# Optimization experiments

Measured on AMD Instinct MI355X. Metric: run time of the kernel, lower is better.

Reference implementation:

```python
import math
import jax, jax.numpy as jnp
import numpy as np

B, T, C = 256, 200, 512
H = 8
N_ATTN = 512
HEAD = N_ATTN // H          # 64
ROT = HEAD // 2             # 32 (rotary_ndims = head_size * 0.5)
MAXLEN = 200
ITEM_NUM = 100000


def setup_inputs() -> dict:
    key = jax.random.key(0)
    ks = jax.random.split(key, 16)
    s = 0.02
    item_emb = jax.random.normal(ks[0], (ITEM_NUM + 1, C), jnp.float32) * s
    item_emb = item_emb.at[0].set(0.0)  # padding_idx=0
    inp = {
        "user_ids": jax.random.randint(ks[1], (B,), 0, 10000),
        "log_seqs": jax.random.randint(ks[2], (B, T), 0, ITEM_NUM + 1),
        "pos_seqs": jax.random.randint(ks[3], (B, T), 0, ITEM_NUM + 1),
        "neg_seqs": jax.random.randint(ks[4], (B, T), 0, ITEM_NUM + 1),
        "item_emb": item_emb,
        "time_w": 1.0 + jax.random.normal(ks[5], (H, MAXLEN), jnp.float32) * 0.1,
        "time_alpha": 1.0 + jax.random.normal(ks[6], (H, 1, MAXLEN), jnp.float32) * 0.1,
        "time_beta": 1.0 + jax.random.normal(ks[7], (H, MAXLEN, 1), jnp.float32) * 0.1,
        "time_gamma": 1.0 + jax.random.normal(ks[8], (MAXLEN, 1), jnp.float32) * 0.1,
        "Wq": jax.random.normal(ks[9], (N_ATTN, C), jnp.float32) * s,
        "bq": jnp.zeros((N_ATTN,), jnp.float32),
        "Wk": jax.random.normal(ks[10], (N_ATTN, C), jnp.float32) * s,
        "bk": jnp.zeros((N_ATTN,), jnp.float32),
        "Wv": jax.random.normal(ks[11], (N_ATTN, C), jnp.float32) * s,
        "bv": jnp.zeros((N_ATTN,), jnp.float32),
        "Wmix": jax.random.normal(ks[12], (H, H), jnp.float32) * (1.0 / math.sqrt(H)),
        "Wo": jax.random.normal(ks[13], (C, N_ATTN), jnp.float32) * s,
        "bo": jnp.zeros((C,), jnp.float32),
    }
    return inp


def _rotate_half(x):
    x1, x2 = x[..., : x.shape[-1] // 2], x[..., x.shape[-1] // 2 :]
    return jnp.concatenate((-x2, x1), axis=-1)


def _mha_pro(x_items, time_w, time_alpha, time_beta, time_gamma,
             Wq, bq, Wk, bk, Wv, bv, Wmix, Wo, bo):
    # x_items: [B, T, C]
    TT = MAXLEN
    # Toeplitz time-decay matrix built exactly like the torch pad/tile/reshape trick
    w = jnp.pad(time_w, ((0, 0), (0, TT)))          # [H, 2TT]
    w = jnp.tile(w, (1, TT))                         # [H, 2TT*TT]
    w = w[:, :-TT].reshape(H, TT, 2 * TT - 1)        # [H, TT, 2TT-1]
    w = w[:, :, TT - 1 :]                            # [H, TT, TT]
    w = w[:, :T, :T] * time_alpha[:, :, :T] * time_beta[:, :T, :]  # [H, T, T]

    # time_shift: shift first half of channels down by one token
    half = C // 2
    shifted = jnp.pad(x_items[:, :, :half], ((0, 0), (1, 0), (0, 0)))[:, :-1]
    x = jnp.concatenate([shifted, x_items[:, :, half:]], axis=-1)  # [B, T, C]

    q = (x @ Wq.T + bq).reshape(B, T, H, HEAD).transpose(0, 2, 1, 3)  # [B,H,T,D]
    k = (x @ Wk.T + bk).reshape(B, T, H, HEAD).transpose(0, 2, 1, 3)
    v = (x @ Wv.T + bv).reshape(B, T, H, HEAD).transpose(0, 2, 1, 3)

    # partial rotary on first ROT dims
    q_rot, q_pass = q[..., :ROT], q[..., ROT:]
    k_rot, k_pass = k[..., :ROT], k[..., ROT:]
    inv_freq = 1.0 / (10000.0 ** (jnp.arange(0, ROT, 2, dtype=jnp.float32) / ROT))
    freqs = jnp.arange(T, dtype=jnp.float32)[:, None] * inv_freq[None, :]  # [T, ROT/2]
    emb = jnp.concatenate((freqs, freqs), axis=-1)   # [T, ROT]
    cos, sin = jnp.cos(emb), jnp.sin(emb)
    q_rot = q_rot * cos + _rotate_half(q_rot) * sin
    k_rot = k_rot * cos + _rotate_half(k_rot) * sin
    q = jnp.concatenate((q_rot, q_pass), axis=-1)
    k = jnp.concatenate((k_rot, k_pass), axis=-1)

    att = jnp.einsum('bhtd,bhsd->bhts', q, k) * (1.0 / math.sqrt(HEAD))
    causal = jnp.tril(jnp.ones((T, T), bool))
    att = jnp.where(causal, att, -jnp.inf)
    att = jax.nn.softmax(att, axis=-1)
    att = att * w                                   # learned time-decay mask
    att = jnp.einsum('hg,bgts->bhts', Wmix, att)    # 1x1 conv across heads

    out = jnp.einsum('bhts,bhsd->bhtd', att, v)
    out = out.transpose(0, 2, 1, 3).reshape(B, T, N_ATTN)
    out = (out @ Wo.T + bo) * time_gamma[:T, :]
    return out


def reference(user_ids, log_seqs, pos_seqs, neg_seqs, item_emb,
              time_w, time_alpha, time_beta, time_gamma,
              Wq, bq, Wk, bk, Wv, bv, Wmix, Wo, bo):
    x_items = item_emb[log_seqs]                    # [B, T, C]
    log_feats = _mha_pro(x_items, time_w, time_alpha, time_beta, time_gamma,
                         Wq, bq, Wk, bk, Wv, bv, Wmix, Wo, bo)
    pos_embs = item_emb[pos_seqs]
    neg_embs = item_emb[neg_seqs]
    pos_logits = log_feats * pos_embs               # [B, T, C] (as in source)
    neg_logits = (log_feats * neg_embs).sum(axis=-1)  # [B, T]
    return pos_logits, neg_logits
```

## Files before the change

kernel.cpp:

```cpp
#include <hip/hip_runtime.h>

#define B_    256
#define T_    200
#define C_    512
#define H_    8
#define HEAD_ 64
#define M_    (B_ * T_)
#define POS_OUT_ (M_ * C_)
#define QK_ROWS_ 208
#define VT_PAD_  224
#define P_PAD_   200

typedef __attribute__((ext_vector_type(8))) _Float16 f16x8;
typedef __attribute__((ext_vector_type(4))) _Float16 f16x4;
typedef __attribute__((ext_vector_type(2))) _Float16 f16x2;
typedef __attribute__((ext_vector_type(4))) float f32x4;

__device__ __forceinline__ void gload16(const void* g, void* l) {
    __builtin_amdgcn_global_load_lds(
        (const __attribute__((address_space(1))) unsigned int*)g,
        (__attribute__((address_space(3))) unsigned int*)l, 16, 0, 0);
}

__global__ __launch_bounds__(256) void gather_shift_k(
    const float* __restrict__ emb, const int* __restrict__ logs,
    _Float16* __restrict__ x)
{
    int bt = blockIdx.x;
    int t  = bt % T_;
    int tid = threadIdx.x;
    int c  = tid * 2;
    _Float16* xr = x + (size_t)bt * C_;
    if (c < 256) {
        if (t == 0) {
            *(f16x2*)(xr + c) = (f16x2){(_Float16)0.0f, (_Float16)0.0f};
        } else {
            int id_prev = logs[bt - 1];
            float2 v = *(const float2*)(emb + (size_t)id_prev * C_ + c);
            *(f16x2*)(xr + c) = (f16x2){(_Float16)v.x, (_Float16)v.y};
        }
    } else {
        int id_cur = logs[bt];
        float2 v = *(const float2*)(emb + (size_t)id_cur * C_ + c);
        *(f16x2*)(xr + c) = (f16x2){(_Float16)v.x, (_Float16)v.y};
    }
}

__global__ __launch_bounds__(256) void convert_w_k(
    const float* __restrict__ Wq, const float* __restrict__ Wk,
    const float* __restrict__ Wv, const float* __restrict__ Wo,
    _Float16* __restrict__ dst)
{
    int idx = blockIdx.x * 256 + threadIdx.x;
    int mat = idx >> 16;
    int off = (idx & 65535) << 2;
    const float* src = (mat == 0) ? Wq : (mat == 1) ? Wk : (mat == 2) ? Wv : Wo;
    float4 v = *(const float4*)(src + off);
    f16x4 o = { (_Float16)v.x, (_Float16)v.y, (_Float16)v.z, (_Float16)v.w };
    *(f16x4*)(dst + ((size_t)mat << 18) + off) = o;
}

__global__ __launch_bounds__(256) void wtab_k(
    const float* __restrict__ tw, const float* __restrict__ ta,
    const float* __restrict__ tb, float* __restrict__ wtab)
{
    int idx = blockIdx.x * 256 + threadIdx.x;
    int g   = idx / (208 * 208);
    int rem = idx % (208 * 208);
    int t = rem / 208, s = rem % 208;
    int tt = min(t, 199), ss = min(s, 199);
    int wi = min(max(199 - tt + ss, 0), 199);
    wtab[idx] = tw[g * 200 + wi] * ta[g * 200 + ss] * tb[g * 200 + tt];
}

__global__ __launch_bounds__(256) void zero_neg_k(float* __restrict__ out)
{
    out[(size_t)POS_OUT_ + blockIdx.x * 256 + threadIdx.x] = 0.0f;
}

__global__ __launch_bounds__(256) void zero_pads_k(
    _Float16* __restrict__ Qb, _Float16* __restrict__ Kb,
    _Float16* __restrict__ Vt)
{
    int bh = blockIdx.x;
    int tid = threadIdx.x;
    for (int idx = tid; idx < 8 * 64; idx += 256) {
        Qb[(size_t)bh * QK_ROWS_ * 64 + 200 * 64 + idx] = (_Float16)0.0f;
        Kb[(size_t)bh * QK_ROWS_ * 64 + 200 * 64 + idx] = (_Float16)0.0f;
    }
    for (int idx = tid; idx < 64 * (VT_PAD_ - 200); idx += 256) {
        int d = idx / (VT_PAD_ - 200), s = 200 + idx % (VT_PAD_ - 200);
        Vt[(size_t)bh * 64 * VT_PAD_ + (size_t)d * VT_PAD_ + s] = (_Float16)0.0f;
    }
}

__global__ __launch_bounds__(256) void gemm_qkv_k(
    const _Float16* __restrict__ xh,
    const _Float16* __restrict__ Wh,
    const float* __restrict__ bq, const float* __restrict__ bk, const float* __restrict__ bv,
    _Float16* __restrict__ Qb, _Float16* __restrict__ Kb,
    _Float16* __restrict__ Vt,
    int nmt)
{
    int n = blockIdx.x;
    int mt, v;
    if ((nmt & 7) == 0) { int q8 = n & 7, i = n >> 3; mt = (i / 12) * 8 + q8; v = i % 12; }
    else               { mt = n / 12; v = n % 12; }
    int which = v >> 2;
    int nt    = v & 3;
    int m0    = mt * 128;
    const _Float16* Wm = Wh + ((size_t)(which * 4 + nt) * 128) * 512;
    const float* bias = (which == 0) ? bq : (which == 1) ? bk : bv;

    __shared__ _Float16 As[3][128 * 32];
    __shared__ _Float16 Bs[3][128 * 32];

    int tid  = threadIdx.x;
    int w    = tid >> 6, lane = tid & 63;
    int quad = lane >> 4, l15 = lane & 15;
    int wm   = w >> 1,    wn  = w & 1;
    int srow = lane >> 2, scg = lane & 3;
    int scg_src = scg ^ ((srow >> 1) & 3);
    int rq = (l15 >> 1) & 3;

    auto stage = [&](int buf, int k0) {
#pragma unroll
        for (int rr = 0; rr < 2; ++rr) {
            int seg = rr * 4 + w;
            int row = seg * 16 + srow;
            gload16(xh + (size_t)(m0 + row) * 512 + k0 + scg_src * 8, As[buf] + seg * 512);
            gload16(Wm + (size_t)row * 512 + k0 + scg_src * 8, Bs[buf] + seg * 512);
        }
    };

    f32x4 acc[4][4];
#pragma unroll
    for (int m = 0; m < 4; ++m)
#pragma unroll
        for (int nn = 0; nn < 4; ++nn) acc[m][nn] = (f32x4){0.f, 0.f, 0.f, 0.f};

    stage(0, 0);
    stage(1, 32);
#pragma unroll
    for (int s = 0; s < 16; ++s) {
        if (s < 15) asm volatile("s_waitcnt vmcnt(4)" ::: "memory");
        else        asm volatile("s_waitcnt vmcnt(0)" ::: "memory");
        __builtin_amdgcn_s_barrier();
        __builtin_amdgcn_sched_barrier(0);
        const _Float16* Ab = As[s % 3];
        const _Float16* Bb = Bs[s % 3];
        f16x8 af[4], bf[4];
#pragma unroll
        for (int m = 0; m < 4; ++m)
            af[m] = *(const f16x8*)(Ab + (wm * 4 + m) * 512 + l15 * 32 + (quad ^ rq) * 8);
#pragma unroll
        for (int nn = 0; nn < 4; ++nn)
            bf[nn] = *(const f16x8*)(Bb + (wn * 4 + nn) * 512 + l15 * 32 + (quad ^ rq) * 8);
        if (s <= 13) stage((s + 2) % 3, (s + 2) * 32);
#pragma unroll
        for (int m = 0; m < 4; ++m)
#pragma unroll
            for (int nn = 0; nn < 4; ++nn)
                acc[m][nn] = __builtin_amdgcn_mfma_f32_16x16x32_f16(af[m], bf[nn], acc[m][nn], 0, 0, 0);
    }

    int h = nt * 2 + wn;
    if (which < 2) {
        _Float16* dst = (which == 0) ? Qb : Kb;
        float sc = (which == 0) ? 0.125f : 1.0f;
        float invf = powf(10000.0f, -(float)l15 / 16.0f);
#pragma unroll
        for (int m = 0; m < 4; ++m) {
#pragma unroll
            for (int r = 0; r < 4; ++r) {
                int row = m0 + wm * 64 + m * 16 + quad * 4 + r;
                int bl = row / T_, t = row % T_;
                float sn, cs;
                __sincosf((float)t * invf, &sn, &cs);
                size_t base = ((size_t)(bl * 8 + h) * QK_ROWS_ + t) * 64;
                float av = acc[m][0][r] + bias[h * 64 + l15];
                float bv2 = acc[m][1][r] + bias[h * 64 + 16 + l15];
                dst[base + l15]      = (_Float16)((av * cs - bv2 * sn) * sc);
                dst[base + 16 + l15] = (_Float16)((bv2 * cs + av * sn) * sc);
                dst[base + 32 + l15] = (_Float16)((acc[m][2][r] + bias[h * 64 + 32 + l15]) * sc);
                dst[base + 48 + l15] = (_Float16)((acc[m][3][r] + bias[h * 64 + 48 + l15]) * sc);
            }
        }
    } else {
#pragma unroll
        for (int nn = 0; nn < 4; ++nn) {
            int ch = nn * 16 + l15;
            float bval = bias[h * 64 + ch];
#pragma unroll
            for (int m = 0; m < 4; ++m) {
                int r0 = m0 + wm * 64 + m * 16 + quad * 4;
                int t0v = r0 % T_;
                if (t0v <= 196) {
                    int bl = r0 / T_;
                    f16x4 v4 = {(_Float16)(acc[m][nn][0] + bval),
                                (_Float16)(acc[m][nn][1] + bval),
                                (_Float16)(acc[m][nn][2] + bval),
                                (_Float16)(acc[m][nn][3] + bval)};
                    *(f16x4*)(Vt + ((size_t)(bl * 8 + h) * 64 + ch) * VT_PAD_ + t0v) = v4;
                } else {
#pragma unroll
                    for (int r = 0; r < 4; ++r) {
                        int rw = r0 + r;
                        int bl = rw / T_, s = rw % T_;
                        Vt[((size_t)(bl * 8 + h) * 64 + ch) * VT_PAD_ + s] = (_Float16)(acc[m][nn][r] + bval);
                    }
                }
            }
        }
    }
}

__global__ __launch_bounds__(512, 4) void attn_fused_k(
    const _Float16* __restrict__ Qb, const _Float16* __restrict__ Kb,
    const _Float16* __restrict__ Vt,
    const float* __restrict__ wtab,
    const float* __restrict__ wmix,
    _Float16* __restrict__ ao)
{
    int n    = blockIdx.x;
    int xcd  = n & 7, slot = n >> 3;
    int i_tile = 12 - (slot % 13);
    int b      = (slot / 13) * 8 + xcd;

    int tid  = threadIdx.x;
    int wave = tid >> 6, lane = tid & 63;
    int quad = lane >> 4, l15 = lane & 15;
    int t0   = i_tile * 16;
    int nst  = i_tile + 1;
    int smax = nst * 16;
    int lim  = smax < 200 ? smax : 200;

    __shared__ _Float16 Pt[8][16][P_PAD_];
    __shared__ float mixs[64];

    if (tid < 64) mixs[tid] = wmix[tid];

    {
        int g = wave;
        const _Float16* Qg = Qb + (size_t)(b * 8 + g) * QK_ROWS_ * 64;
        const _Float16* Kg = Kb + (size_t)(b * 8 + g) * QK_ROWS_ * 64;
        f16x8 a0 = *(const f16x8*)(Qg + (size_t)(t0 + l15) * 64 + quad * 8);
        f16x8 a1 = *(const f16x8*)(Qg + (size_t)(t0 + l15) * 64 + quad * 8 + 32);

        f32x4 sf[13];
        __builtin_amdgcn_s_setprio(1);
#pragma unroll
        for (int st = 0; st < 13; ++st) if (st < nst) {
            f16x8 k0 = *(const f16x8*)(Kg + (size_t)(st * 16 + l15) * 64 + quad * 8);
            f16x8 k1 = *(const f16x8*)(Kg + (size_t)(st * 16 + l15) * 64 + quad * 8 + 32);
            f32x4 c = {0.f, 0.f, 0.f, 0.f};
            c = __builtin_amdgcn_mfma_f32_16x16x32_f16(a0, k0, c, 0, 0, 0);
            c = __builtin_amdgcn_mfma_f32_16x16x32_f16(a1, k1, c, 0, 0, 0);
            sf[st] = c;
        }
        __builtin_amdgcn_s_setprio(0);
        float inv[4];
#pragma unroll
        for (int r = 0; r < 4; ++r) {
            int t = t0 + quad * 4 + r;
            float sum = 0.f;
#pragma unroll
            for (int st = 0; st < 13; ++st) {
                if (st < nst - 1) {
                    float e = __expf(sf[st][r]); sf[st][r] = e; sum += e;
                } else if (st == nst - 1) {
                    int s = t0 + l15;
                    float e = (s <= t) ? __expf(sf[st][r]) : 0.f;
                    sf[st][r] = e; sum += e;
                }
            }
            sum += __shfl_xor(sum, 1);
            sum += __shfl_xor(sum, 2);
            sum += __shfl_xor(sum, 4);
            sum += __shfl_xor(sum, 8);
            inv[r] = 1.0f / sum;
        }
        const float* wg = wtab + ((size_t)g * 208 + t0) * 208;
#pragma unroll
        for (int st = 0; st < 13; ++st) if (st < nst) {
            int s = st * 16 + l15;
#pragma unroll
            for (int r = 0; r < 4; ++r) {
                int trow = quad * 4 + r;
                float wv = wg[trow * 208 + s];
                if (s < 200)
                    Pt[g][trow][s] = (_Float16)(sf[st][r] * inv[r] * wv);
            }
        }
    }
    __syncthreads();

    {
        f16x2 mx[64];
#pragma unroll
        for (int i = 0; i < 64; ++i) {
            _Float16 mh = (_Float16)mixs[i];
            mx[i] = (f16x2){mh, mh};
        }
        int nitems = lim << 3;
        for (int idx = tid; idx < nitems; idx += 512) {
            int tloc = idx & 15;
            int sp   = (idx >> 4) << 1;
            f16x2 pv[8];
#pragma unroll
            for (int g = 0; g < 8; ++g) pv[g] = *(const f16x2*)&Pt[g][tloc][sp];
#pragma unroll
            for (int ho = 0; ho < 8; ++ho) {
                f16x2 o = mx[ho * 8] * pv[0];
#pragma unroll
                for (int g = 1; g < 8; ++g) o += mx[ho * 8 + g] * pv[g];
                *(f16x2*)&Pt[ho][tloc][sp] = o;
            }
        }
    }
    __syncthreads();

    {
        int nk = (nst + 1) >> 1;
        int hda = wave;
        const _Float16* Vh = Vt + (size_t)(b * 8 + hda) * 64 * VT_PAD_;
        f32x4 c4[4];
#pragma unroll
        for (int n2 = 0; n2 < 4; ++n2) c4[n2] = (f32x4){0.f, 0.f, 0.f, 0.f};
        __builtin_amdgcn_s_setprio(1);
#pragma unroll
        for (int ks = 0; ks < 7; ++ks) if (ks < nk) {
            int cc = ks * 32 + quad * 8;
            bool oob = cc >= lim;
            int cl = oob ? 0 : cc;
            f16x8 a = *(const f16x8*)(&Pt[hda][l15][cl]);
            if (oob) {
#pragma unroll
                for (int j = 0; j < 8; ++j) a[j] = (_Float16)0.0f;
            }
#pragma unroll
            for (int n2 = 0; n2 < 4; ++n2) {
                f16x8 bb = *(const f16x8*)(Vh + (size_t)(n2 * 16 + l15) * VT_PAD_ + ks * 32 + quad * 8);
                c4[n2] = __builtin_amdgcn_mfma_f32_16x16x32_f16(a, bb, c4[n2], 0, 0, 0);
            }
        }
        __builtin_amdgcn_s_setprio(0);
#pragma unroll
        for (int n2 = 0; n2 < 4; ++n2)
#pragma unroll
            for (int r = 0; r < 4; ++r) {
                int t = t0 + quad * 4 + r;
                if (t < 200)
                    ao[((size_t)(b * T_ + t)) * 512 + hda * 64 + n2 * 16 + l15] = (_Float16)c4[n2][r];
            }
    }
}

__global__ __launch_bounds__(256) void gemm_out_k(
    const _Float16* __restrict__ Ah, const _Float16* __restrict__ Woh,
    const float* __restrict__ bo, const float* __restrict__ gamma,
    const float* __restrict__ emb, const int* __restrict__ pos,
    const int* __restrict__ neg, float* __restrict__ out,
    int bt0, int nmt)
{
    int n = blockIdx.x;
    int mt, nt;
    if ((nmt & 7) == 0) { int q8 = n & 7, i = n >> 3; mt = (i / 4) * 8 + q8; nt = i % 4; }
    else               { mt = n / 4; nt = n % 4; }
    int m0 = mt * 128;
    const _Float16* Wm = Woh + (size_t)nt * 128 * 512;

    __shared__ _Float16 As[3][128 * 32];
    __shared__ _Float16 Bs[3][128 * 32];

    int tid  = threadIdx.x;
    int w    = tid >> 6, lane = tid & 63;
    int quad = lane >> 4, l15 = lane & 15;
    int wm   = w >> 1,    wn  = w & 1;
    int srow = lane >> 2, scg = lane & 3;
    int scg_src = scg ^ ((srow >> 1) & 3);
    int rq = (l15 >> 1) & 3;

    auto stage = [&](int buf, int k0) {
#pragma unroll
        for (int rr = 0; rr < 2; ++rr) {
            int seg = rr * 4 + w;
            int row = seg * 16 + srow;
            gload16(Ah + (size_t)(m0 + row) * 512 + k0 + scg_src * 8, As[buf] + seg * 512);
            gload16(Wm + (size_t)row * 512 + k0 + scg_src * 8, Bs[buf] + seg * 512);
        }
    };

    f32x4 acc[4][4];
#pragma unroll
    for (int m = 0; m < 4; ++m)
#pragma unroll
        for (int nn = 0; nn < 4; ++nn) acc[m][nn] = (f32x4){0.f, 0.f, 0.f, 0.f};

    stage(0, 0);
    stage(1, 32);
#pragma unroll
    for (int s = 0; s < 16; ++s) {
        if (s < 15) asm volatile("s_waitcnt vmcnt(4)" ::: "memory");
        else        asm volatile("s_waitcnt vmcnt(0)" ::: "memory");
        __builtin_amdgcn_s_barrier();
        __builtin_amdgcn_sched_barrier(0);
        const _Float16* Ab = As[s % 3];
        const _Float16* Bb = Bs[s % 3];
        f16x8 af[4], bf[4];
#pragma unroll
        for (int m = 0; m < 4; ++m)
            af[m] = *(const f16x8*)(Ab + (wm * 4 + m) * 512 + l15 * 32 + (quad ^ rq) * 8);
#pragma unroll
        for (int nn = 0; nn < 4; ++nn)
            bf[nn] = *(const f16x8*)(Bb + (wn * 4 + nn) * 512 + l15 * 32 + (quad ^ rq) * 8);
        if (s <= 13) stage((s + 2) % 3, (s + 2) * 32);
#pragma unroll
        for (int m = 0; m < 4; ++m)
#pragma unroll
            for (int nn = 0; nn < 4; ++nn)
                acc[m][nn] = __builtin_amdgcn_mfma_f32_16x16x32_f16(af[m], bf[nn], acc[m][nn], 0, 0, 0);
    }

#pragma unroll
    for (int m = 0; m < 4; ++m) {
#pragma unroll
        for (int r = 0; r < 4; ++r) {
            int row = m0 + wm * 64 + m * 16 + quad * 4 + r;
            float gg = gamma[row % T_];
            int pr = pos[row], nr = neg[row];
            const float* pe = emb + (size_t)pr * 512;
            const float* ne = emb + (size_t)nr * 512;
            float* po = out + (size_t)(bt0 + row) * 512;
            float s = 0.f;
#pragma unroll
            for (int nn = 0; nn < 4; ++nn) {
                int col = nt * 128 + wn * 64 + nn * 16 + l15;
                float val = (acc[m][nn][r] + bo[col]) * gg;
                po[col] = val * pe[col];
                s += val * ne[col];
            }
            s += __shfl_xor(s, 1);
            s += __shfl_xor(s, 2);
            s += __shfl_xor(s, 4);
            s += __shfl_xor(s, 8);
            if (l15 == 0)
                atomicAdd(out + (size_t)POS_OUT_ + bt0 + row, s);
        }
    }
}

extern "C" void kernel_launch(void* const* d_in, const int* in_sizes, int n_in,
                              void* d_out, int out_size, void* d_ws, size_t ws_size,
                              hipStream_t stream)
{
    const int* logs = (const int*)d_in[1];
    const int* pos  = (const int*)d_in[2];
    const int* neg  = (const int*)d_in[3];
    const float* emb = (const float*)d_in[4];
    const float* tw  = (const float*)d_in[5];
    const float* ta  = (const float*)d_in[6];
    const float* tb  = (const float*)d_in[7];
    const float* tg  = (const float*)d_in[8];
    const float* Wq  = (const float*)d_in[9];
    const float* bq  = (const float*)d_in[10];
    const float* Wk  = (const float*)d_in[11];
    const float* bk  = (const float*)d_in[12];
    const float* Wv  = (const float*)d_in[13];
    const float* bv  = (const float*)d_in[14];
    const float* wmix= (const float*)d_in[15];
    const float* Wo  = (const float*)d_in[16];
    const float* bo  = (const float*)d_in[17];

    const size_t PER_B = (size_t)T_ * C_ * 2
                       + (size_t)8 * QK_ROWS_ * 64 * 2
                       + (size_t)8 * QK_ROWS_ * 64 * 2
                       + (size_t)8 * 64 * VT_PAD_ * 2
                       + (size_t)T_ * C_ * 2;
    const size_t SZ_WH = (size_t)4 * 512 * 512 * 2;
    const size_t SZ_WT = (size_t)8 * 208 * 208 * 4;

    int CB = (ws_size >= SZ_WH + SZ_WT + PER_B * B_) ? B_ : 32;
    int nch = B_ / CB;
    int CM = CB * T_;
    int NMT = CM / 128;

    char* p = (char*)d_ws;
    _Float16*       Wh   = (_Float16*)p;  p += SZ_WH;
    float*          wtab = (float*)p;     p += SZ_WT;
    _Float16*       xh   = (_Float16*)p;  p += (size_t)CM * C_ * 2;
    _Float16*       Qb   = (_Float16*)p;  p += (size_t)CB * 8 * QK_ROWS_ * 64 * 2;
    _Float16*       Kb   = (_Float16*)p;  p += (size_t)CB * 8 * QK_ROWS_ * 64 * 2;
    _Float16*       Vt   = (_Float16*)p;  p += (size_t)CB * 8 * 64 * VT_PAD_ * 2;
    _Float16*       aoh  = (_Float16*)p;

    convert_w_k<<<1024, 256, 0, stream>>>(Wq, Wk, Wv, Wo, Wh);
    wtab_k<<<1352, 256, 0, stream>>>(tw, ta, tb, wtab);
    zero_neg_k<<<M_ / 256, 256, 0, stream>>>((float*)d_out);
    zero_pads_k<<<CB * 8, 256, 0, stream>>>(Qb, Kb, Vt);

    for (int c = 0; c < nch; ++c) {
        int bt0 = c * CM;
        gather_shift_k<<<CM, 256, 0, stream>>>(emb, logs + bt0, xh);
        gemm_qkv_k<<<NMT * 12, 256, 0, stream>>>(xh, Wh, bq, bk, bv, Qb, Kb, Vt, NMT);
        attn_fused_k<<<13 * CB, 512, 0, stream>>>(Qb, Kb, Vt, wtab, wmix, aoh);
        gemm_out_k<<<NMT * 4, 256, 0, stream>>>(aoh, Wh + (size_t)3 * 512 * 512, bo, tg,
                                                emb, pos + bt0, neg + bt0, (float*)d_out, bt0, NMT);
    }
}
```

Before: 680.5 us.

## Pipeline K/V loads in attention, defer softmax normalization, vectorize gather kernel

In the attention kernel, the QK^T loop now prefetches the K tiles and time-decay weights two steps ahead in rotating registers. It also computes exp, the running row sums and the weighted P stores inside the same loop, instead of keeping all 13 score tiles live. The 1/sum normalization is stored per row in shared memory as fp16 and applied during the head-mixing stage. The PV stage double-buffers V fragments in registers. The gather kernel becomes a grid-stride loop with float4 loads over a fixed 2048-block grid. This cuts register pressure and exposed load latency, but it changes rounding: unnormalized exp values are stored in fp16. The gather loop bound uses the full M_ rows rather than the chunk size.

```diff
diff --git a/kernel.cpp b/kernel.cpp
--- a/kernel.cpp
+++ b/kernel.cpp
@@ -26,23 +26,23 @@
     const float* __restrict__ emb, const int* __restrict__ logs,
     _Float16* __restrict__ x)
 {
-    int bt = blockIdx.x;
-    int t  = bt % T_;
-    int tid = threadIdx.x;
-    int c  = tid * 2;
-    _Float16* xr = x + (size_t)bt * C_;
-    if (c < 256) {
-        if (t == 0) {
-            *(f16x2*)(xr + c) = (f16x2){(_Float16)0.0f, (_Float16)0.0f};
+    const int total = M_ * 128;
+    for (int gid = blockIdx.x * 256 + threadIdx.x; gid < total; gid += gridDim.x * 256) {
+        int bt = gid >> 7;
+        int c  = (gid & 127) * 4;
+        int t  = bt % T_;
+        _Float16* xr = x + (size_t)bt * C_ + c;
+        if (c < 256) {
+            if (t == 0) {
+                *(f16x4*)xr = (f16x4){(_Float16)0.f, (_Float16)0.f, (_Float16)0.f, (_Float16)0.f};
+                continue;
+            }
+            float4 v = *(const float4*)(emb + (size_t)logs[bt - 1] * C_ + c);
+            *(f16x4*)xr = (f16x4){(_Float16)v.x, (_Float16)v.y, (_Float16)v.z, (_Float16)v.w};
         } else {
-            int id_prev = logs[bt - 1];
-            float2 v = *(const float2*)(emb + (size_t)id_prev * C_ + c);
-            *(f16x2*)(xr + c) = (f16x2){(_Float16)v.x, (_Float16)v.y};
-        }
-    } else {
-        int id_cur = logs[bt];
-        float2 v = *(const float2*)(emb + (size_t)id_cur * C_ + c);
-        *(f16x2*)(xr + c) = (f16x2){(_Float16)v.x, (_Float16)v.y};
+            float4 v = *(const float4*)(emb + (size_t)logs[bt] * C_ + c);
+            *(f16x4*)xr = (f16x4){(_Float16)v.x, (_Float16)v.y, (_Float16)v.z, (_Float16)v.w};
+        }
     }
 }
 
@@ -237,59 +237,70 @@
 
     __shared__ _Float16 Pt[8][16][P_PAD_];
     __shared__ float mixs[64];
+    __shared__ f16x2 invt[8][16];
 
     if (tid < 64) mixs[tid] = wmix[tid];
 
     {
         int g = wave;
+        int trow = quad * 4;
         const _Float16* Qg = Qb + (size_t)(b * 8 + g) * QK_ROWS_ * 64;
         const _Float16* Kg = Kb + (size_t)(b * 8 + g) * QK_ROWS_ * 64;
         f16x8 a0 = *(const f16x8*)(Qg + (size_t)(t0 + l15) * 64 + quad * 8);
         f16x8 a1 = *(const f16x8*)(Qg + (size_t)(t0 + l15) * 64 + quad * 8 + 32);
-
-        f32x4 sf[13];
+        const float* wg = wtab + ((size_t)g * 208 + t0) * 208;
+
+        f16x8 kr0[3], kr1[3];
+        float wr[3][4];
+        kr0[0] = *(const f16x8*)(Kg + (size_t)l15 * 64 + quad * 8);
+        kr1[0] = *(const f16x8*)(Kg + (size_t)l15 * 64 + quad * 8 + 32);
+#pragma unroll
+        for (int r = 0; r < 4; ++r) wr[0][r] = wg[(trow + r) * 208 + l15];
+        if (nst > 1) {
+            kr0[1] = *(const f16x8*)(Kg + (size_t)(16 + l15) * 64 + quad * 8);
+            kr1[1] = *(const f16x8*)(Kg + (size_t)(16 + l15) * 64 + quad * 8 + 32);
+#pragma unroll
+            for (int r = 0; r < 4; ++r) wr[1][r] = wg[(trow + r) * 208 + 16 + l15];
+        }
+        __builtin_amdgcn_sched_barrier(0);
+
+        float sum[4] = {0.f, 0.f, 0.f, 0.f};
         __builtin_amdgcn_s_setprio(1);
 #pragma unroll
         for (int st = 0; st < 13; ++st) if (st < nst) {
-            f16x8 k0 = *(const f16x8*)(Kg + (size_t)(st * 16 + l15) * 64 + quad * 8);
-            f16x8 k1 = *(const f16x8*)(Kg + (size_t)(st * 16 + l15) * 64 + quad * 8 + 32);
+            if (st + 2 < nst) {
+                int sl = (st + 2) % 3;
+                kr0[sl] = *(const f16x8*)(Kg + (size_t)((st + 2) * 16 + l15) * 64 + quad * 8);
+                kr1[sl] = *(const f16x8*)(Kg + (size_t)((st + 2) * 16 + l15) * 64 + quad * 8 + 32);
+#pragma unroll
+                for (int r = 0; r < 4; ++r) wr[sl][r] = wg[(trow + r) * 208 + (st + 2) * 16 + l15];
+                __builtin_amdgcn_sched_barrier(0);
+            }
+            int cl = st % 3;
             f32x4 c = {0.f, 0.f, 0.f, 0.f};
-            c = __builtin_amdgcn_mfma_f32_16x16x32_f16(a0, k0, c, 0, 0, 0);
-            c = __builtin_amdgcn_mfma_f32_16x16x32_f16(a1, k1, c, 0, 0, 0);
-            sf[st] = c;
+            c = __builtin_amdgcn_mfma_f32_16x16x32_f16(a0, kr0[cl], c, 0, 0, 0);
+            c = __builtin_amdgcn_mfma_f32_16x16x32_f16(a1, kr1[cl], c, 0, 0, 0);
+            int s = st * 16 + l15;
+            bool diag = (st == nst - 1);
+#pragma unroll
+            for (int r = 0; r < 4; ++r) {
+                int t = t0 + trow + r;
+                float e = (!diag || s <= t) ? __expf(c[r]) : 0.f;
+                sum[r] += e;
+                if (s < 200) Pt[g][trow + r][s] = (_Float16)(e * wr[cl][r]);
+            }
         }
         __builtin_amdgcn_s_setprio(0);
-        float inv[4];
 #pragma unroll
         for (int r = 0; r < 4; ++r) {
-            int t = t0 + quad * 4 + r;
-            float sum = 0.f;
-#pragma unroll
-            for (int st = 0; st < 13; ++st) {
-                if (st < nst - 1) {
-                    float e = __expf(sf[st][r]); sf[st][r] = e; sum += e;
-                } else if (st == nst - 1) {
-                    int s = t0 + l15;
-                    float e = (s <= t) ? __expf(sf[st][r]) : 0.f;
-                    sf[st][r] = e; sum += e;
-                }
-            }
-            sum += __shfl_xor(sum, 1);
-            sum += __shfl_xor(sum, 2);
-            sum += __shfl_xor(sum, 4);
-            sum += __shfl_xor(sum, 8);
-            inv[r] = 1.0f / sum;
-        }
-        const float* wg = wtab + ((size_t)g * 208 + t0) * 208;
-#pragma unroll
-        for (int st = 0; st < 13; ++st) if (st < nst) {
-            int s = st * 16 + l15;
-#pragma unroll
-            for (int r = 0; r < 4; ++r) {
-                int trow = quad * 4 + r;
-                float wv = wg[trow * 208 + s];
-                if (s < 200)
-                    Pt[g][trow][s] = (_Float16)(sf[st][r] * inv[r] * wv);
+            float sm = sum[r];
+            sm += __shfl_xor(sm, 1);
+            sm += __shfl_xor(sm, 2);
+            sm += __shfl_xor(sm, 4);
+            sm += __shfl_xor(sm, 8);
+            if (l15 == 0) {
+                _Float16 ih = (_Float16)(1.0f / sm);
+                invt[g][trow + r] = (f16x2){ih, ih};
             }
         }
     }
@@ -310,6 +321,8 @@
 #pragma unroll
             for (int g = 0; g < 8; ++g) pv[g] = *(const f16x2*)&Pt[g][tloc][sp];
 #pragma unroll
+            for (int g = 0; g < 8; ++g) pv[g] = pv[g] * invt[g][tloc];
+#pragma unroll
             for (int ho = 0; ho < 8; ++ho) {
                 f16x2 o = mx[ho * 8] * pv[0];
 #pragma unroll
@@ -327,9 +340,19 @@
         f32x4 c4[4];
 #pragma unroll
         for (int n2 = 0; n2 < 4; ++n2) c4[n2] = (f32x4){0.f, 0.f, 0.f, 0.f};
+        f16x8 vb[2][4];
+#pragma unroll
+        for (int n2 = 0; n2 < 4; ++n2)
+            vb[0][n2] = *(const f16x8*)(Vh + (size_t)(n2 * 16 + l15) * VT_PAD_ + quad * 8);
         __builtin_amdgcn_s_setprio(1);
 #pragma unroll
         for (int ks = 0; ks < 7; ++ks) if (ks < nk) {
+            if (ks + 1 < nk) {
+#pragma unroll
+                for (int n2 = 0; n2 < 4; ++n2)
+                    vb[(ks + 1) & 1][n2] = *(const f16x8*)(Vh + (size_t)(n2 * 16 + l15) * VT_PAD_ + (ks + 1) * 32 + quad * 8);
+                __builtin_amdgcn_sched_barrier(0);
+            }
             int cc = ks * 32 + quad * 8;
             bool oob = cc >= lim;
             int cl = oob ? 0 : cc;
@@ -339,10 +362,8 @@
                 for (int j = 0; j < 8; ++j) a[j] = (_Float16)0.0f;
             }
 #pragma unroll
-            for (int n2 = 0; n2 < 4; ++n2) {
-                f16x8 bb = *(const f16x8*)(Vh + (size_t)(n2 * 16 + l15) * VT_PAD_ + ks * 32 + quad * 8);
-                c4[n2] = __builtin_amdgcn_mfma_f32_16x16x32_f16(a, bb, c4[n2], 0, 0, 0);
-            }
+            for (int n2 = 0; n2 < 4; ++n2)
+                c4[n2] = __builtin_amdgcn_mfma_f32_16x16x32_f16(a, vb[ks & 1][n2], c4[n2], 0, 0, 0);
         }
         __builtin_amdgcn_s_setprio(0);
 #pragma unroll
@@ -501,7 +522,7 @@
 
     for (int c = 0; c < nch; ++c) {
         int bt0 = c * CM;
-        gather_shift_k<<<CM, 256, 0, stream>>>(emb, logs + bt0, xh);
+        gather_shift_k<<<2048, 256, 0, stream>>>(emb, logs + bt0, xh);
         gemm_qkv_k<<<NMT * 12, 256, 0, stream>>>(xh, Wh, bq, bk, bv, Qb, Kb, Vt, NMT);
         attn_fused_k<<<13 * CB, 512, 0, stream>>>(Qb, Kb, Vt, wtab, wmix, aoh);
         gemm_out_k<<<NMT * 4, 256, 0, stream>>>(aoh, Wh + (size_t)3 * 512 * 512, bo, tg,
```

Measured after the change: 664.4 us (median of 2 runs). 2.4% less time.
